# Kernel optimization log

Measured on AMD Instinct MI355X. Metric: run time of the kernel, lower is better.

Reference implementation:

```python
import jax, jax.numpy as jnp
import numpy as np

IN_FEATURES = 1024
OUT_FEATURES = 1024
GRID_SIZE = 5
SPLINE_ORDER = 3
GRID_RANGE = (-1.0, 1.0)


def make_grid():
    h = (GRID_RANGE[1] - GRID_RANGE[0]) / GRID_SIZE
    g = jnp.arange(-SPLINE_ORDER, GRID_SIZE + SPLINE_ORDER + 1, dtype=jnp.float32) * h + GRID_RANGE[0]
    return jnp.tile(g[None, :], (IN_FEATURES, 1))  # (in, G + 2k + 1)


def b_splines(x, grid):
    # x: (N, in), grid: (in, G+2k+1) -> bases: (N, in, G+k)
    xe = x[..., None]
    bases = ((xe >= grid[:, :-1]) & (xe < grid[:, 1:])).astype(x.dtype)
    for k in range(1, SPLINE_ORDER + 1):
        left = (xe - grid[:, :-(k + 1)]) / (grid[:, k:-1] - grid[:, :-(k + 1)])
        right = (grid[:, k + 1:] - xe) / (grid[:, k + 1:] - grid[:, 1:-k])
        bases = left * bases[:, :, :-1] + right * bases[:, :, 1:]
    return bases


def setup_inputs() -> dict:
    key = jax.random.key(0)
    k1, k2, k3 = jax.random.split(key, 3)
    x = jax.random.uniform(k1, (8192, IN_FEATURES), dtype=jnp.float32)
    # lecun_normal-style init: std = 1/sqrt(fan_in)
    base_weight = jax.random.normal(k2, (OUT_FEATURES, IN_FEATURES), dtype=jnp.float32) / np.sqrt(IN_FEATURES)
    coeff = GRID_SIZE + SPLINE_ORDER
    spline_weight = jax.random.normal(k3, (OUT_FEATURES, IN_FEATURES, coeff), dtype=jnp.float32) / np.sqrt(IN_FEATURES * coeff)
    spline_scaler = jnp.ones((OUT_FEATURES, IN_FEATURES), dtype=jnp.float32)
    grid = make_grid()
    return {"x": x, "grid": grid, "base_weight": base_weight,
            "spline_weight": spline_weight, "spline_scaler": spline_scaler}


def reference(x, grid, base_weight, spline_weight, spline_scaler):
    N = x.shape[0]
    base_out = jax.nn.silu(x) @ base_weight.T  # (N, out)
    bases = b_splines(x, grid)                 # (N, in, G+k)
    scaled_sw = spline_weight * spline_scaler[..., None]  # (out, in, G+k)
    spline_out = bases.reshape(N, -1) @ scaled_sw.reshape(OUT_FEATURES, -1).T  # (N, out)
    return base_out + spline_out
```

## Files before the change

kernel.cpp:

```cpp
#include <hip/hip_runtime.h>
#include <hip/hip_bf16.h>

#define IN_F 1024
#define OUT_F 1024
#define KTOT (IN_F * 9)
#define M_ROWS 8192

#define BM 256
#define BN 128
#define BK 64
#define NT (KTOT / BK)

typedef short bf16x8 __attribute__((ext_vector_type(8)));
typedef int   i32x4  __attribute__((ext_vector_type(4)));
typedef float f32x4  __attribute__((ext_vector_type(4)));

#define AS1 __attribute__((address_space(1)))
#define AS3 __attribute__((address_space(3)))

__device__ __forceinline__ void kan_basis_fast(
    float xv, const float* __restrict__ g,
    const float* __restrict__ inv1, const float* __restrict__ inv2,
    const float* __restrict__ inv3, float* __restrict__ out) {
  float b[11];
#pragma unroll
  for (int j = 0; j < 11; ++j)
    b[j] = (xv >= g[j] && xv < g[j + 1]) ? 1.0f : 0.0f;
#pragma unroll
  for (int j = 0; j < 10; ++j)
    b[j] = (xv - g[j]) * inv1[j] * b[j] + (g[j + 2] - xv) * inv1[j + 1] * b[j + 1];
#pragma unroll
  for (int j = 0; j < 9; ++j)
    b[j] = (xv - g[j]) * inv2[j] * b[j] + (g[j + 3] - xv) * inv2[j + 1] * b[j + 1];
#pragma unroll
  for (int j = 0; j < 8; ++j)
    b[j] = (xv - g[j]) * inv3[j] * b[j] + (g[j + 4] - xv) * inv3[j + 1] * b[j + 1];
#pragma unroll
  for (int j = 0; j < 8; ++j) out[j] = b[j];
}

__global__ __launch_bounds__(256) void expand_a(
    const float* __restrict__ x, const float* __restrict__ grid,
    __hip_bfloat16* __restrict__ A, int row0, int nrows) {
  int t = blockIdx.x * 256 + threadIdx.x;
  int n = t >> 7;
  if (n >= nrows) return;
  int i0 = (t & 127) * 8;

  float g[12];
  const float* gp = grid + (size_t)i0 * 12;
#pragma unroll
  for (int j = 0; j < 12; ++j) g[j] = gp[j];
  float inv1[11], inv2[10], inv3[9];
#pragma unroll
  for (int j = 0; j < 11; ++j) inv1[j] = 1.0f / (g[j + 1] - g[j]);
#pragma unroll
  for (int j = 0; j < 10; ++j) inv2[j] = 1.0f / (g[j + 2] - g[j]);
#pragma unroll
  for (int j = 0; j < 9; ++j)  inv3[j] = 1.0f / (g[j + 3] - g[j]);

  const float* xp = x + (size_t)(row0 + n) * IN_F + i0;
  float xs[8];
  *(f32x4*)&xs[0] = *(const f32x4*)xp;
  *(f32x4*)&xs[4] = *(const f32x4*)(xp + 4);

  bf16x8 out[9];
#pragma unroll
  for (int j = 0; j < 8; ++j) {
    float xv = xs[j];
    float bas[8];
    kan_basis_fast(xv, g, inv1, inv2, inv3, bas);
    float s = xv / (1.0f + __expf(-xv));
    out[0][j] = (short)__bfloat16_as_ushort(__float2bfloat16(s));
#pragma unroll
    for (int c = 0; c < 8; ++c)
      out[c + 1][j] = (short)__bfloat16_as_ushort(__float2bfloat16(bas[c]));
  }
  __hip_bfloat16* dst = A + (size_t)n * KTOT + i0;
#pragma unroll
  for (int c = 0; c < 9; ++c)
    *(bf16x8*)(dst + (size_t)c * IN_F) = out[c];
}

__global__ __launch_bounds__(256) void pack_b(
    const float* __restrict__ bw, const float* __restrict__ sw,
    const float* __restrict__ sc, __hip_bfloat16* __restrict__ B) {
  int t = blockIdx.x * 256 + threadIdx.x;
  if (t >= OUT_F * 128) return;
  int o = t >> 7;
  int i0 = (t & 127) * 8;

  float bwv[8], scv[8];
  const float* bp = bw + (size_t)o * IN_F + i0;
  const float* sp = sc + (size_t)o * IN_F + i0;
  *(f32x4*)&bwv[0] = *(const f32x4*)bp;
  *(f32x4*)&bwv[4] = *(const f32x4*)(bp + 4);
  *(f32x4*)&scv[0] = *(const f32x4*)sp;
  *(f32x4*)&scv[4] = *(const f32x4*)(sp + 4);

  bf16x8 out[9];
#pragma unroll
  for (int j = 0; j < 8; ++j) {
    out[0][j] = (short)__bfloat16_as_ushort(__float2bfloat16(bwv[j]));
    const float* swp = sw + ((size_t)o * IN_F + i0 + j) * 8;
    float swv[8];
    *(f32x4*)&swv[0] = *(const f32x4*)swp;
    *(f32x4*)&swv[4] = *(const f32x4*)(swp + 4);
#pragma unroll
    for (int c = 0; c < 8; ++c)
      out[c + 1][j] = (short)__bfloat16_as_ushort(__float2bfloat16(swv[c] * scv[j]));
  }
  __hip_bfloat16* dst = B + (size_t)o * KTOT + i0;
#pragma unroll
  for (int c = 0; c < 9; ++c)
    *(bf16x8*)(dst + (size_t)c * IN_F) = out[c];
}


__device__ __forceinline__ void gld16(const __hip_bfloat16* g, __hip_bfloat16* l) {
  __builtin_amdgcn_global_load_lds((AS1 void*)g, (AS3 void*)l, 16, 0, 0);
}

__device__ __forceinline__ bf16x8 dsr128(uint32_t addr) {
  i32x4 r;
  asm volatile("ds_read_b128 %0, %1" : "=v"(r) : "v"(addr));
  return __builtin_bit_cast(bf16x8, r);
}

#define SB __builtin_amdgcn_sched_barrier(0)

#define READ_FRAGS(dA, dB, slot, h) do {                                   \
    uint32_t aS_ = aBase + (uint32_t)(slot) * (BM * BK * 2);               \
    uint32_t bS_ = bBase + (uint32_t)(slot) * (BN * BK * 2);               \
    _Pragma("unroll")                                                      \
    for (int m_ = 0; m_ < 8; ++m_) dA[m_] = dsr128(aS_ + aOffB[h][m_]);    \
    _Pragma("unroll")                                                      \
    for (int n_ = 0; n_ < 4; ++n_) dB[n_] = dsr128(bS_ + bOffB[h][n_]);    \
  } while (0)

#define MFMA_BURST(sA, sB) do {                                            \
    __builtin_amdgcn_s_setprio(1);                                         \
    _Pragma("unroll")                                                      \
    for (int m_ = 0; m_ < 8; ++m_)                                         \
      _Pragma("unroll")                                                    \
      for (int n_ = 0; n_ < 4; ++n_)                                       \
        acc[m_][n_] = __builtin_amdgcn_mfma_f32_16x16x32_bf16(             \
            sA[m_], sB[n_], acc[m_][n_], 0, 0, 0);                         \
    __builtin_amdgcn_s_setprio(0);                                         \
  } while (0)

#define STAGE_T(slot, koff) do {                                           \
    __hip_bfloat16* asD_ = &As[slot][0];                                   \
    __hip_bfloat16* bsD_ = &Bs[slot][0];                                   \
    _Pragma("unroll")                                                      \
    for (int j_ = 0; j_ < 8; ++j_)                                         \
      gld16(aSrc0 + (size_t)j_ * 32 * KTOT + (koff), asD_ + j_ * 2048 + wv * 512); \
    _Pragma("unroll")                                                      \
    for (int j_ = 0; j_ < 4; ++j_)                                         \
      gld16(bSrc0 + (size_t)j_ * 32 * KTOT + (koff), bsD_ + j_ * 2048 + wv * 512); \
  } while (0)

__global__ __launch_bounds__(256, 1) void gemm_v6(
    const __hip_bfloat16* __restrict__ A, const __hip_bfloat16* __restrict__ B,
    float* __restrict__ C) {
  __shared__ __align__(16) __hip_bfloat16 As[3][BM * BK];
  __shared__ __align__(16) __hip_bfloat16 Bs[3][BN * BK];

  const int nwg = gridDim.x;
  const int q = nwg >> 3;
  const int L = (blockIdx.x & 7) * q + (blockIdx.x >> 3);
  const int bm = L >> 3, bn = L & 7;

  const int tid = threadIdx.x;
  const int lane = tid & 63;
  const int wv = tid >> 6;
  const int wm = wv >> 1;
  const int wn = wv & 1;
  const int l15 = lane & 15, lhi = lane >> 4;

  const int srow = wv * 8 + (lane >> 3);
  const int scol = ((lane & 7) ^ ((lane >> 3) & 7)) * 8;
  const __hip_bfloat16* aSrc0 = A + (size_t)(bm * BM + srow) * KTOT + scol;
  const __hip_bfloat16* bSrc0 = B + (size_t)(bn * BN + srow) * KTOT + scol;

  const uint32_t aBase = (uint32_t)(uintptr_t)(AS3 const void*)&As[0][0];
  const uint32_t bBase = (uint32_t)(uintptr_t)(AS3 const void*)&Bs[0][0];
  uint32_t aOffB[2][8], bOffB[2][4];
#pragma unroll
  for (int h = 0; h < 2; ++h) {
#pragma unroll
    for (int m = 0; m < 8; ++m) {
      int rowA = wm * 128 + m * 16 + l15;
      aOffB[h][m] = (rowA * 64 + (((h * 4 + lhi) ^ (l15 & 7)) * 8)) * 2;
    }
#pragma unroll
    for (int n = 0; n < 4; ++n) {
      int rowB = wn * 64 + n * 16 + l15;
      bOffB[h][n] = (rowB * 64 + (((h * 4 + lhi) ^ (l15 & 7)) * 8)) * 2;
    }
  }

  f32x4 acc[8][4];
#pragma unroll
  for (int m = 0; m < 8; ++m)
#pragma unroll
    for (int n = 0; n < 4; ++n) acc[m][n] = f32x4{0.f, 0.f, 0.f, 0.f};

  bf16x8 fa[8], fb[4];
  bf16x8 ga[8], gb[4];

  STAGE_T(0, 0);
  STAGE_T(1, BK);
  asm volatile("s_waitcnt vmcnt(12)" ::: "memory");
  SB;
  __builtin_amdgcn_s_barrier();
  SB;
  READ_FRAGS(fa, fb, 0, 0);
  SB;

  int cur = 0;
  for (int t = 0; t < NT - 2; ++t) {
    const int nxt = cur == 2 ? 0 : cur + 1;
    const int stg = cur == 0 ? 2 : cur - 1;
    READ_FRAGS(ga, gb, cur, 1);
    STAGE_T(stg, (t + 2) * BK);
    SB;
    asm volatile("s_waitcnt lgkmcnt(12)" ::: "memory");
    SB;
    MFMA_BURST(fa, fb);
    SB;
    asm volatile("s_waitcnt lgkmcnt(0)" ::: "memory");
    SB;
    asm volatile("s_waitcnt vmcnt(12)" ::: "memory");
    SB;
    __builtin_amdgcn_s_barrier();
    SB;
    READ_FRAGS(fa, fb, nxt, 0);
    SB;
    MFMA_BURST(ga, gb);
    SB;
    cur = nxt;
  }
  {
    const int nxt = cur == 2 ? 0 : cur + 1;
    READ_FRAGS(ga, gb, cur, 1);
    SB;
    asm volatile("s_waitcnt lgkmcnt(12)" ::: "memory");
    SB;
    MFMA_BURST(fa, fb);
    SB;
    asm volatile("s_waitcnt lgkmcnt(0)" ::: "memory");
    SB;
    asm volatile("s_waitcnt vmcnt(0)" ::: "memory");
    SB;
    __builtin_amdgcn_s_barrier();
    SB;
    READ_FRAGS(fa, fb, nxt, 0);
    SB;
    MFMA_BURST(ga, gb);
    SB;
    cur = nxt;
  }
  {
    READ_FRAGS(ga, gb, cur, 1);
    SB;
    asm volatile("s_waitcnt lgkmcnt(12)" ::: "memory");
    SB;
    MFMA_BURST(fa, fb);
    SB;
    asm volatile("s_waitcnt lgkmcnt(0)" ::: "memory");
    SB;
    MFMA_BURST(ga, gb);
    SB;
  }

#pragma unroll
  for (int m = 0; m < 8; ++m)
#pragma unroll
    for (int n = 0; n < 4; ++n) {
      int col = bn * BN + wn * 64 + n * 16 + l15;
      int row0 = bm * BM + wm * 128 + m * 16 + lhi * 4;
#pragma unroll
      for (int j = 0; j < 4; ++j)
        C[(size_t)(row0 + j) * OUT_F + col] = acc[m][n][j];
    }
}

__global__ __launch_bounds__(256) void kan_naive(
    const float* __restrict__ x, const float* __restrict__ grid,
    const float* __restrict__ bw, const float* __restrict__ sw,
    const float* __restrict__ sc, float* __restrict__ out) {
  __shared__ float s_act[IN_F];
  __shared__ float s_bas[IN_F * 8];
  int n = blockIdx.x;
  for (int i = threadIdx.x; i < IN_F; i += 256) {
    float xv = x[(size_t)n * IN_F + i];
    float g[12];
    const float* gp = grid + i * 12;
#pragma unroll
    for (int t = 0; t < 12; ++t) g[t] = gp[t];
    float b[11];
#pragma unroll
    for (int j = 0; j < 11; ++j)
      b[j] = (xv >= g[j] && xv < g[j + 1]) ? 1.0f : 0.0f;
#pragma unroll
    for (int k = 1; k <= 3; ++k)
#pragma unroll
      for (int j = 0; j < 11 - k; ++j) {
        float left = (xv - g[j]) / (g[j + k] - g[j]);
        float right = (g[j + k + 1] - xv) / (g[j + k + 1] - g[j + 1]);
        b[j] = left * b[j] + right * b[j + 1];
      }
    s_act[i] = xv / (1.0f + __expf(-xv));
#pragma unroll
    for (int c = 0; c < 8; ++c) s_bas[i * 8 + c] = b[c];
  }
  __syncthreads();
  for (int o = threadIdx.x; o < OUT_F; o += 256) {
    float acc = 0.f;
    const float* bwo = bw + (size_t)o * IN_F;
    const float* swo = sw + (size_t)o * IN_F * 8;
    const float* sco = sc + (size_t)o * IN_F;
    for (int i = 0; i < IN_F; ++i) {
      acc += s_act[i] * bwo[i];
      float p = 0.f;
#pragma unroll
      for (int c = 0; c < 8; ++c) p += s_bas[i * 8 + c] * swo[i * 8 + c];
      acc += p * sco[i];
    }
    out[(size_t)n * OUT_F + o] = acc;
  }
}

extern "C" void kernel_launch(void* const* d_in, const int* in_sizes, int n_in,
                              void* d_out, int out_size, void* d_ws, size_t ws_size,
                              hipStream_t stream) {
  const float* x  = (const float*)d_in[0];
  const float* grid = (const float*)d_in[1];
  const float* bw = (const float*)d_in[2];
  const float* sw = (const float*)d_in[3];
  const float* sc = (const float*)d_in[4];
  float* out = (float*)d_out;

  const size_t Bbytes = (size_t)OUT_F * KTOT * 2;
  const size_t rowBytes = (size_t)KTOT * 2;

  if (ws_size >= Bbytes + 256 * rowBytes) {
    __hip_bfloat16* Bp = (__hip_bfloat16*)d_ws;
    __hip_bfloat16* Ap = (__hip_bfloat16*)((char*)d_ws + Bbytes);
    size_t arows = (ws_size - Bbytes) / rowBytes;
    int chunk = (int)((arows / 256) * 256);
    if (chunk > M_ROWS) chunk = M_ROWS;

    pack_b<<<OUT_F * 128 / 256, 256, 0, stream>>>(bw, sw, sc, Bp);
    for (int r0 = 0; r0 < M_ROWS; r0 += chunk) {
      int rows = M_ROWS - r0 < chunk ? M_ROWS - r0 : chunk;
      expand_a<<<(rows * 128 + 255) / 256, 256, 0, stream>>>(x, grid, Ap, r0, rows);
      gemm_v6<<<(rows / BM) * 8, 256, 0, stream>>>(Ap, Bp, out + (size_t)r0 * OUT_F);
    }
  } else {
    kan_naive<<<M_ROWS, 256, 0, stream>>>(x, grid, bw, sw, sc, out);
  }
}
```

Baseline: 204.6 us.

## Split GEMM workgroup into eight waves with smaller per-wave tiles

The GEMM block tile (256x128) now runs on 512 threads (8 waves), so each wave computes a 64x64 sub-tile with a 4x4 accumulator instead of 8x4. Global-to-LDS staging is redistributed across 8 waves, and the wait counts are adjusted to the smaller per-wave load counts. The goal is more waves per CU to hide latency and lower register pressure per wave. In exchange, each wave reuses fewer fragments per LDS read, and barrier synchronisation covers more waves.

```diff
diff --git a/kernel.cpp b/kernel.cpp
--- a/kernel.cpp
+++ b/kernel.cpp
@@ -133,7 +133,7 @@
     uint32_t aS_ = aBase + (uint32_t)(slot) * (BM * BK * 2);               \
     uint32_t bS_ = bBase + (uint32_t)(slot) * (BN * BK * 2);               \
     _Pragma("unroll")                                                      \
-    for (int m_ = 0; m_ < 8; ++m_) dA[m_] = dsr128(aS_ + aOffB[h][m_]);    \
+    for (int m_ = 0; m_ < 4; ++m_) dA[m_] = dsr128(aS_ + aOffB[h][m_]);    \
     _Pragma("unroll")                                                      \
     for (int n_ = 0; n_ < 4; ++n_) dB[n_] = dsr128(bS_ + bOffB[h][n_]);    \
   } while (0)
@@ -141,7 +141,7 @@
 #define MFMA_BURST(sA, sB) do {                                            \
     __builtin_amdgcn_s_setprio(1);                                         \
     _Pragma("unroll")                                                      \
-    for (int m_ = 0; m_ < 8; ++m_)                                         \
+    for (int m_ = 0; m_ < 4; ++m_)                                         \
       _Pragma("unroll")                                                    \
       for (int n_ = 0; n_ < 4; ++n_)                                       \
         acc[m_][n_] = __builtin_amdgcn_mfma_f32_16x16x32_bf16(             \
@@ -153,14 +153,14 @@
     __hip_bfloat16* asD_ = &As[slot][0];                                   \
     __hip_bfloat16* bsD_ = &Bs[slot][0];                                   \
     _Pragma("unroll")                                                      \
-    for (int j_ = 0; j_ < 8; ++j_)                                         \
-      gld16(aSrc0 + (size_t)j_ * 32 * KTOT + (koff), asD_ + j_ * 2048 + wv * 512); \
-    _Pragma("unroll")                                                      \
     for (int j_ = 0; j_ < 4; ++j_)                                         \
-      gld16(bSrc0 + (size_t)j_ * 32 * KTOT + (koff), bsD_ + j_ * 2048 + wv * 512); \
+      gld16(aSrc[j_] + (koff), asD_ + aDst[j_]);                           \
+    _Pragma("unroll")                                                      \
+    for (int j_ = 0; j_ < 2; ++j_)                                         \
+      gld16(bSrc[j_] + (koff), bsD_ + bDst[j_]);                           \
   } while (0)
 
-__global__ __launch_bounds__(256, 1) void gemm_v6(
+__global__ __launch_bounds__(512, 2) void gemm_v7(
     const __hip_bfloat16* __restrict__ A, const __hip_bfloat16* __restrict__ B,
     float* __restrict__ C) {
   __shared__ __align__(16) __hip_bfloat16 As[3][BM * BK];
@@ -177,41 +177,53 @@
   const int wm = wv >> 1;
   const int wn = wv & 1;
   const int l15 = lane & 15, lhi = lane >> 4;
-
-  const int srow = wv * 8 + (lane >> 3);
-  const int scol = ((lane & 7) ^ ((lane >> 3) & 7)) * 8;
-  const __hip_bfloat16* aSrc0 = A + (size_t)(bm * BM + srow) * KTOT + scol;
-  const __hip_bfloat16* bSrc0 = B + (size_t)(bn * BN + srow) * KTOT + scol;
+  const int K = KTOT;
+
+  const __hip_bfloat16* aSrc[4];
+  const __hip_bfloat16* bSrc[2];
+  int aDst[4], bDst[2];
+#pragma unroll
+  for (int j = 0; j < 4; ++j) {
+    int p = j * 512 + wv * 64 + lane;
+    int row = p >> 3;
+    int col = (p & 7) ^ (row & 7);
+    aSrc[j] = A + (size_t)(bm * BM + row) * K + col * 8;
+    aDst[j] = (j * 512 + wv * 64) * 8;
+  }
+#pragma unroll
+  for (int j = 0; j < 2; ++j) {
+    int p = j * 512 + wv * 64 + lane;
+    int row = p >> 3;
+    int col = (p & 7) ^ (row & 7);
+    bSrc[j] = B + (size_t)(bn * BN + row) * K + col * 8;
+    bDst[j] = (j * 512 + wv * 64) * 8;
+  }
 
   const uint32_t aBase = (uint32_t)(uintptr_t)(AS3 const void*)&As[0][0];
   const uint32_t bBase = (uint32_t)(uintptr_t)(AS3 const void*)&Bs[0][0];
-  uint32_t aOffB[2][8], bOffB[2][4];
-#pragma unroll
-  for (int h = 0; h < 2; ++h) {
-#pragma unroll
-    for (int m = 0; m < 8; ++m) {
-      int rowA = wm * 128 + m * 16 + l15;
+  uint32_t aOffB[2][4], bOffB[2][4];
+#pragma unroll
+  for (int h = 0; h < 2; ++h)
+#pragma unroll
+    for (int m = 0; m < 4; ++m) {
+      int rowA = wm * 64 + m * 16 + l15;
       aOffB[h][m] = (rowA * 64 + (((h * 4 + lhi) ^ (l15 & 7)) * 8)) * 2;
+      int rowB = wn * 64 + m * 16 + l15;
+      bOffB[h][m] = (rowB * 64 + (((h * 4 + lhi) ^ (l15 & 7)) * 8)) * 2;
     }
-#pragma unroll
-    for (int n = 0; n < 4; ++n) {
-      int rowB = wn * 64 + n * 16 + l15;
-      bOffB[h][n] = (rowB * 64 + (((h * 4 + lhi) ^ (l15 & 7)) * 8)) * 2;
-    }
-  }
-
-  f32x4 acc[8][4];
-#pragma unroll
-  for (int m = 0; m < 8; ++m)
+
+  f32x4 acc[4][4];
+#pragma unroll
+  for (int m = 0; m < 4; ++m)
 #pragma unroll
     for (int n = 0; n < 4; ++n) acc[m][n] = f32x4{0.f, 0.f, 0.f, 0.f};
 
-  bf16x8 fa[8], fb[4];
-  bf16x8 ga[8], gb[4];
+  bf16x8 fa[4], fb[4];
+  bf16x8 ga[4], gb[4];
 
   STAGE_T(0, 0);
   STAGE_T(1, BK);
-  asm volatile("s_waitcnt vmcnt(12)" ::: "memory");
+  asm volatile("s_waitcnt vmcnt(6)" ::: "memory");
   SB;
   __builtin_amdgcn_s_barrier();
   SB;
@@ -225,13 +237,13 @@
     READ_FRAGS(ga, gb, cur, 1);
     STAGE_T(stg, (t + 2) * BK);
     SB;
-    asm volatile("s_waitcnt lgkmcnt(12)" ::: "memory");
+    asm volatile("s_waitcnt lgkmcnt(8)" ::: "memory");
     SB;
     MFMA_BURST(fa, fb);
     SB;
     asm volatile("s_waitcnt lgkmcnt(0)" ::: "memory");
     SB;
-    asm volatile("s_waitcnt vmcnt(12)" ::: "memory");
+    asm volatile("s_waitcnt vmcnt(6)" ::: "memory");
     SB;
     __builtin_amdgcn_s_barrier();
     SB;
@@ -245,7 +257,7 @@
     const int nxt = cur == 2 ? 0 : cur + 1;
     READ_FRAGS(ga, gb, cur, 1);
     SB;
-    asm volatile("s_waitcnt lgkmcnt(12)" ::: "memory");
+    asm volatile("s_waitcnt lgkmcnt(8)" ::: "memory");
     SB;
     MFMA_BURST(fa, fb);
     SB;
@@ -264,7 +276,7 @@
   {
     READ_FRAGS(ga, gb, cur, 1);
     SB;
-    asm volatile("s_waitcnt lgkmcnt(12)" ::: "memory");
+    asm volatile("s_waitcnt lgkmcnt(8)" ::: "memory");
     SB;
     MFMA_BURST(fa, fb);
     SB;
@@ -275,11 +287,11 @@
   }
 
 #pragma unroll
-  for (int m = 0; m < 8; ++m)
+  for (int m = 0; m < 4; ++m)
 #pragma unroll
     for (int n = 0; n < 4; ++n) {
       int col = bn * BN + wn * 64 + n * 16 + l15;
-      int row0 = bm * BM + wm * 128 + m * 16 + lhi * 4;
+      int row0 = bm * BM + wm * 64 + m * 16 + lhi * 4;
 #pragma unroll
       for (int j = 0; j < 4; ++j)
         C[(size_t)(row0 + j) * OUT_F + col] = acc[m][n][j];
@@ -356,7 +368,7 @@
     for (int r0 = 0; r0 < M_ROWS; r0 += chunk) {
       int rows = M_ROWS - r0 < chunk ? M_ROWS - r0 : chunk;
       expand_a<<<(rows * 128 + 255) / 256, 256, 0, stream>>>(x, grid, Ap, r0, rows);
-      gemm_v6<<<(rows / BM) * 8, 256, 0, stream>>>(Ap, Bp, out + (size_t)r0 * OUT_F);
+      gemm_v7<<<(rows / BM) * 8, 512, 0, stream>>>(Ap, Bp, out + (size_t)r0 * OUT_F);
     }
   } else {
     kan_naive<<<M_ROWS, 256, 0, stream>>>(x, grid, bw, sw, sc, out);
```

Result: faster. 187.7 us (-8.3%).
